# Kernel optimization log

Measured on AMD Instinct MI355X. Metric: run time of the kernel, lower is better.

Reference implementation:

```python
import jax, jax.numpy as jnp
import numpy as np

B = 512
C = 256
HEADS = 16
DH = 16
SIGMA = 1e-4  # GaussianNoise(0.0001)
LEAK = 0.2


def _axial_attn(x, Wq, Wkv, Wo, bo, axis):
    # x: [B, 8, 4, 5, C]; attend along `axis`, folding other dims into batch.
    xm = jnp.moveaxis(x, axis, -2)                      # [..., T, C]
    q = xm @ Wq                                          # [..., T, C]
    kv = xm @ Wkv                                        # [..., T, 2C]
    k, v = kv[..., :C], kv[..., C:]
    hshape = q.shape[:-1] + (HEADS, DH)
    q = q.reshape(hshape)
    k = k.reshape(hshape)
    v = v.reshape(hshape)
    dots = jnp.einsum('...thd,...shd->...hts', q, k) * (DH ** -0.5)
    attn = jax.nn.softmax(dots, axis=-1)
    o = jnp.einsum('...hts,...shd->...thd', attn, v).reshape(xm.shape)
    o = o @ Wo + bo
    return jnp.moveaxis(o, -2, axis)


def setup_inputs() -> dict:
    key = jax.random.key(0)
    ks = jax.random.split(key, 12)
    inp = {
        'x': jax.random.normal(ks[0], (B, 8, 4, 5), jnp.float32),
        'noise': jax.random.normal(ks[1], (B, 8, 4, 5, 1), jnp.float32),
        'rand': jax.random.uniform(ks[2], (B, 8, 4, 5, 1), jnp.float32),
        # encoder Linear(2, 256, bias=False), stored as [in, out]
        'W_enc': jax.random.normal(ks[3], (2, C), jnp.float32) * (2 ** -0.5),
        # axial positional embedding (sum of per-axis params == one full param)
        'pos_emb': jax.random.normal(ks[4], (8, 4, 5, C), jnp.float32) * 0.02,
        # 2 AxialAttention layers x 3 axes of SelfAttention params
        'Wq': jax.random.normal(ks[5], (2, 3, C, C), jnp.float32) * (C ** -0.5),
        'Wkv': jax.random.normal(ks[6], (2, 3, C, 2 * C), jnp.float32) * (C ** -0.5),
        'Wo': jax.random.normal(ks[7], (2, 3, C, C), jnp.float32) * (C ** -0.5),
        'bo': jnp.zeros((2, 3, C), jnp.float32),
        # decoder Linear(256, 1, bias=True)
        'Wd': jax.random.normal(ks[8], (C, 1), jnp.float32) * (C ** -0.5),
        'bd': jnp.zeros((1,), jnp.float32),
    }
    return inp


def reference(x, noise, rand, W_enc, pos_emb, Wq, Wkv, Wo, bo, Wd, bd):
    h = x[..., None] + SIGMA * noise                  # unsqueeze + GaussianNoise
    h = jnp.concatenate([h, rand], axis=-1)           # [B,8,4,5,2]
    h = jnp.tanh(h @ W_enc)                           # [B,8,4,5,256]
    h = h + pos_emb                                   # axial positional embedding
    for l in range(2):                                # two AxialAttention blocks
        h = (_axial_attn(h, Wq[l, 0], Wkv[l, 0], Wo[l, 0], bo[l, 0], 1)
             + _axial_attn(h, Wq[l, 1], Wkv[l, 1], Wo[l, 1], bo[l, 1], 2)
             + _axial_attn(h, Wq[l, 2], Wkv[l, 2], Wo[l, 2], bo[l, 2], 3))
        h = jnp.where(h >= 0, h, LEAK * h)            # LeakyReLU(0.2)
    out = jax.nn.sigmoid(h @ Wd + bd)                 # decoder Linear + Sigmoid
    return out[..., 0]                                # squeeze(-1) -> [B,8,4,5]
```

## Files before the change

### kernel.cpp

```cpp
#include <hip/hip_runtime.h>
#include <hip/hip_bf16.h>
#include <math.h>

#define NPOS 81920
#define CDIM 256
#define SIGMA 1e-4f
#define LEAK 0.2f

typedef __hip_bfloat16 bf16;
typedef __bf16 bf16x8 __attribute__((ext_vector_type(8)));
typedef float f32x4 __attribute__((ext_vector_type(4)));

__device__ __forceinline__ float bf2f(unsigned short u) {
    return __uint_as_float(((unsigned)u) << 16);
}
__device__ __forceinline__ unsigned short f2bfu(float f) {
    bf16 h = __float2bfloat16(f);
    return *reinterpret_cast<unsigned short*>(&h);
}

__global__ void encode_kernel(const float* __restrict__ x, const float* __restrict__ noise,
                              const float* __restrict__ rnd, const float* __restrict__ We,
                              const float* __restrict__ pe, bf16* __restrict__ H) {
    int p = blockIdx.x;
    int c = threadIdx.x;
    float a = x[p] + SIGMA * noise[p];
    float b = rnd[p];
    float z = a * We[c] + b * We[CDIM + c];
    z = fminf(15.f, fmaxf(-15.f, z));
    float e = __expf(2.f * z);
    float th = 1.f - 2.f / (e + 1.f);
    H[(size_t)p * CDIM + c] = __float2bfloat16(th + pe[(p % 160) * CDIM + c]);
}

__global__ void bias3_kernel(const float* __restrict__ bo, float* __restrict__ bsum) {
    int l = blockIdx.x, c = threadIdx.x;
    bsum[l * CDIM + c] = bo[l * 768 + c] + bo[l * 768 + 256 + c] + bo[l * 768 + 512 + c];
}

__global__ void pack_qkv_kernel(const float* __restrict__ Wq, const float* __restrict__ Wkv,
                                bf16* __restrict__ out) {
    int mat = blockIdx.x / 768;
    int n = blockIdx.x % 768;
    int k = threadIdx.x;
    float v = (n < 256) ? Wq[(size_t)mat * 65536 + (size_t)k * 256 + n]
                        : Wkv[(size_t)mat * 131072 + (size_t)k * 512 + (n - 256)];
    out[(size_t)blockIdx.x * 256 + k] = __float2bfloat16(v);
}
__global__ void pack_wo_kernel(const float* __restrict__ Wo, bf16* __restrict__ out) {
    int l = blockIdx.x / 256;
    int n = blockIdx.x % 256;
    int ck = threadIdx.x;
    for (int a = 0; a < 3; a++)
        out[(size_t)(l * 256 + n) * 768 + a * 256 + ck] =
            __float2bfloat16(Wo[(((size_t)(l * 3 + a)) * 256 + ck) * 256 + n]);
}

__global__ __launch_bounds__(256, 2) void step_kernel(
    const bf16* __restrict__ Hg, const bf16* __restrict__ Wqkv, bf16* __restrict__ QKV,
    const bf16* __restrict__ O, const bf16* __restrict__ WoTl, bf16* __restrict__ Hnw,
    const float* __restrict__ bias, int nW, int nMblk) {
    __shared__ __bf16 smem[32768];
    int tid = threadIdx.x;
    int wave = tid >> 6, lane = tid & 63;
    int quad = lane >> 4, m = lane & 15;

    if (blockIdx.x >= nW) {
        __bf16* As = smem;
        __bf16* Bs = smem + 8192;
        int bid = blockIdx.x - nW;
        int xcd = bid & 7, slot = bid >> 3;
        int g = slot / 9;
        int nb = slot - g * 9;
        int mb = xcd + 8 * g;
        int bm = mb * 128, bn = nb * 256;
        int wr = (wave >> 1) * 64, wc = (wave & 1) * 128;
        f32x4 acc[4][8] = {};

#define STAGE_G(buf, k0)                                                                       \
    {                                                                                          \
        _Pragma("unroll") for (int rep = 0; rep < 2; rep++) {                                  \
            int ch = rep * 256 + wave * 64 + lane;                                             \
            int row = ch >> 2, cc = ch & 3, gc = cc ^ ((row >> 1) & 3);                        \
            __builtin_amdgcn_global_load_lds(                                                  \
                (const __attribute__((address_space(1))) void*)(Hg + (size_t)(bm + row) * CDIM \
                                                                + (k0) + gc * 8),              \
                (__attribute__((address_space(3))) void*)(As + (buf) * 4096                    \
                                                          + (rep * 256 + wave * 64) * 8),      \
                16, 0, 0);                                                                     \
        }                                                                                      \
        _Pragma("unroll") for (int rep = 0; rep < 4; rep++) {                                  \
            int ch = rep * 256 + wave * 64 + lane;                                             \
            int row = ch >> 2, cc = ch & 3, gc = cc ^ ((row >> 1) & 3);                        \
            __builtin_amdgcn_global_load_lds(                                                  \
                (const __attribute__((address_space(1))) void*)(Wqkv + (size_t)(bn + row) * 256\
                                                                + (k0) + gc * 8),              \
                (__attribute__((address_space(3))) void*)(Bs + (buf) * 8192                    \
                                                          + (rep * 256 + wave * 64) * 8),      \
                16, 0, 0);                                                                     \
        }                                                                                      \
    }

        STAGE_G(0, 0);
#pragma unroll
        for (int it = 0; it < 8; it++) {
            __syncthreads();
            if (it < 7) STAGE_G((it + 1) & 1, (it + 1) * 32);
            const __bf16* Ab = As + (it & 1) * 4096;
            const __bf16* Bb = Bs + (it & 1) * 8192;
            bf16x8 af[4], bfr[8];
#pragma unroll
            for (int i = 0; i < 4; i++) {
                int r = wr + i * 16 + m;
                af[i] = *(const bf16x8*)(Ab + r * 32 + ((quad ^ ((r >> 1) & 3)) * 8));
            }
#pragma unroll
            for (int j = 0; j < 8; j++) {
                int r = wc + j * 16 + m;
                bfr[j] = *(const bf16x8*)(Bb + r * 32 + ((quad ^ ((r >> 1) & 3)) * 8));
            }
#pragma unroll
            for (int i = 0; i < 4; i++)
#pragma unroll
                for (int j = 0; j < 8; j++)
                    acc[i][j] = __builtin_amdgcn_mfma_f32_16x16x32_bf16(af[i], bfr[j], acc[i][j], 0, 0, 0);
        }
#undef STAGE_G

        __syncthreads();
        {
            unsigned short* ct = (unsigned short*)smem;
#pragma unroll
            for (int i = 0; i < 4; i++)
#pragma unroll
                for (int j = 0; j < 8; j++)
#pragma unroll
                    for (int r = 0; r < 4; r++) {
                        int row = wr + i * 16 + quad * 4 + r;
                        int col = wc + j * 16 + m;
                        ct[row * 256 + col] = f2bfu(acc[i][j][r]);
                    }
            __syncthreads();
#pragma unroll
            for (int p = 0; p < 16; p++) {
                int chunk = p * 256 + tid;
                int row = chunk >> 5, c8 = (chunk & 31) * 8;
                ulonglong2 v = *(const ulonglong2*)(ct + row * 256 + c8);
                *(ulonglong2*)((unsigned short*)QKV + (size_t)(bm + row) * 2304 + bn + c8) = v;
            }
        }
    } else {
        __bf16* As = smem;
        __bf16* Bs = smem + 16384;
        int bid = blockIdx.x;
        int xcd = bid & 7, slot = bid >> 3;
        int g = slot >> 1;
        int nb = slot & 1;
        int mb = xcd + 8 * g;
        int bm = mb * 128, bn = nb * 128;
        int wr = (wave >> 1) * 64, wc = (wave & 1) * 64;
        f32x4 acc[4][4] = {};

#define STAGE_W(buf, k0)                                                                       \
    {                                                                                          \
        _Pragma("unroll") for (int rep = 0; rep < 4; rep++) {                                  \
            int ch = rep * 256 + wave * 64 + lane;                                             \
            int row = ch >> 3, cc = ch & 7, gc = cc ^ (row & 7);                               \
            __builtin_amdgcn_global_load_lds(                                                  \
                (const __attribute__((address_space(1))) void*)(O + (size_t)(bm + row) * 768   \
                                                                + (k0) + gc * 8),              \
                (__attribute__((address_space(3))) void*)(As + (buf) * 8192                    \
                                                          + (rep * 256 + wave * 64) * 8),      \
                16, 0, 0);                                                                     \
        }                                                                                      \
        _Pragma("unroll") for (int rep = 0; rep < 4; rep++) {                                  \
            int ch = rep * 256 + wave * 64 + lane;                                             \
            int row = ch >> 3, cc = ch & 7, gc = cc ^ (row & 7);                               \
            __builtin_amdgcn_global_load_lds(                                                  \
                (const __attribute__((address_space(1))) void*)(WoTl + (size_t)(bn + row) * 768\
                                                                + (k0) + gc * 8),              \
                (__attribute__((address_space(3))) void*)(Bs + (buf) * 8192                    \
                                                          + (rep * 256 + wave * 64) * 8),      \
                16, 0, 0);                                                                     \
        }                                                                                      \
    }

        STAGE_W(0, 0);
#pragma unroll
        for (int it = 0; it < 12; it++) {
            __syncthreads();
            if (it < 11) STAGE_W((it + 1) & 1, (it + 1) * 64);
            const __bf16* Ab = As + (it & 1) * 8192;
            const __bf16* Bb = Bs + (it & 1) * 8192;
#pragma unroll
            for (int kk = 0; kk < 2; kk++) {
                bf16x8 af[4], bfr[4];
#pragma unroll
                for (int i = 0; i < 4; i++) {
                    int r = wr + i * 16 + m, cix = kk * 4 + quad;
                    af[i] = *(const bf16x8*)(Ab + r * 64 + ((cix ^ (r & 7)) * 8));
                }
#pragma unroll
                for (int j = 0; j < 4; j++) {
                    int r = wc + j * 16 + m, cix = kk * 4 + quad;
                    bfr[j] = *(const bf16x8*)(Bb + r * 64 + ((cix ^ (r & 7)) * 8));
                }
#pragma unroll
                for (int i = 0; i < 4; i++)
#pragma unroll
                    for (int j = 0; j < 4; j++)
                        acc[i][j] = __builtin_amdgcn_mfma_f32_16x16x32_bf16(af[i], bfr[j], acc[i][j], 0, 0, 0);
            }
        }
#undef STAGE_W

        __syncthreads();
        {
            unsigned short* ct = (unsigned short*)smem;
#pragma unroll
            for (int i = 0; i < 4; i++)
#pragma unroll
                for (int j = 0; j < 4; j++)
#pragma unroll
                    for (int r = 0; r < 4; r++) {
                        int row = wr + i * 16 + quad * 4 + r;
                        int lcol = wc + j * 16 + m;
                        float v = acc[i][j][r] + bias[bn + lcol];
                        v = v >= 0.f ? v : LEAK * v;
                        ct[row * 128 + lcol] = f2bfu(v);
                    }
            __syncthreads();
#pragma unroll
            for (int p = 0; p < 8; p++) {
                int chunk = p * 256 + tid;
                int row = chunk >> 4, c8 = (chunk & 15) * 8;
                ulonglong2 v = *(const ulonglong2*)(ct + row * 128 + c8);
                *(ulonglong2*)((unsigned short*)Hnw + (size_t)(bm + row) * CDIM + bn + c8) = v;
            }
        }
    }
}

template <int AXIS>
__device__ __forceinline__ void attn_axis(const bf16* __restrict__ QKV, bf16* __restrict__ O,
                                          int seq, int lane) {
    constexpr int T      = (AXIS == 0) ? 8 : (AXIS == 1) ? 4 : 5;
    constexpr int STRIDE = (AXIS == 0) ? 20 : (AXIS == 1) ? 5 : 1;
    int base;
    if (AXIS == 0)      { int b = seq / 20, r = seq % 20; base = b * 160 + r; }
    else if (AXIS == 1) { int b = seq / 40, r = seq % 40; base = b * 160 + (r / 5) * 20 + (r % 5); }
    else                { int b = seq / 32, r = seq % 32; base = b * 160 + r * 5; }

    float q[T][4], k[T][4], v[T][4];
#pragma unroll
    for (int t = 0; t < T; t++) {
        const unsigned short* rowp =
            (const unsigned short*)QKV + (size_t)(base + t * STRIDE) * 2304 + AXIS * 768 + lane * 4;
        ushort4 qu = *(const ushort4*)(rowp);
        ushort4 ku = *(const ushort4*)(rowp + 256);
        ushort4 vu = *(const ushort4*)(rowp + 512);
        q[t][0] = bf2f(qu.x); q[t][1] = bf2f(qu.y); q[t][2] = bf2f(qu.z); q[t][3] = bf2f(qu.w);
        k[t][0] = bf2f(ku.x); k[t][1] = bf2f(ku.y); k[t][2] = bf2f(ku.z); k[t][3] = bf2f(ku.w);
        v[t][0] = bf2f(vu.x); v[t][1] = bf2f(vu.y); v[t][2] = bf2f(vu.z); v[t][3] = bf2f(vu.w);
    }

#pragma unroll
    for (int t = 0; t < T; t++) {
        float sc[T];
#pragma unroll
        for (int s = 0; s < T; s++) {
            float p = q[t][0] * k[s][0] + q[t][1] * k[s][1] + q[t][2] * k[s][2] + q[t][3] * k[s][3];
            p += __shfl_xor(p, 1);
            p += __shfl_xor(p, 2);
            sc[s] = p * 0.25f;
        }
        float mx = sc[0];
#pragma unroll
        for (int s = 1; s < T; s++) mx = fmaxf(mx, sc[s]);
        float sum = 0.f;
#pragma unroll
        for (int s = 0; s < T; s++) { sc[s] = __expf(sc[s] - mx); sum += sc[s]; }
        float inv = 1.f / sum;
        float o0 = 0.f, o1 = 0.f, o2 = 0.f, o3 = 0.f;
#pragma unroll
        for (int s = 0; s < T; s++) {
            o0 += sc[s] * v[s][0]; o1 += sc[s] * v[s][1];
            o2 += sc[s] * v[s][2]; o3 += sc[s] * v[s][3];
        }
        ushort4 st;
        st.x = f2bfu(o0 * inv); st.y = f2bfu(o1 * inv);
        st.z = f2bfu(o2 * inv); st.w = f2bfu(o3 * inv);
        *(ushort4*)((unsigned short*)O + (size_t)(base + t * STRIDE) * 768 + AXIS * 256 + lane * 4) = st;
    }
}

__global__ __launch_bounds__(256) void attn_all(const bf16* __restrict__ QKV,
                                                bf16* __restrict__ O, int n0, int n1) {
    int wave = threadIdx.x >> 6, lane = threadIdx.x & 63;
    int blk = blockIdx.x;
    if (blk < n0)            attn_axis<0>(QKV, O, blk * 4 + wave, lane);
    else if (blk < n0 + n1)  attn_axis<1>(QKV, O, (blk - n0) * 4 + wave, lane);
    else                     attn_axis<2>(QKV, O, (blk - n0 - n1) * 4 + wave, lane);
}

__global__ void decode_kernel(const bf16* __restrict__ H, const float* __restrict__ Wd,
                              const float* __restrict__ bd, float* __restrict__ out) {
    int tid = threadIdx.x;
    int pos = blockIdx.x * 4 + (tid >> 6);
    int lane = tid & 63;
    float acc = 0.f;
#pragma unroll
    for (int q = 0; q < 4; q++) {
        int c = lane + q * 64;
        acc += __bfloat162float(H[(size_t)pos * CDIM + c]) * Wd[c];
    }
#pragma unroll
    for (int off = 32; off > 0; off >>= 1) acc += __shfl_down(acc, off);
    if (lane == 0) out[pos] = 1.f / (1.f + __expf(-(acc + bd[0])));
}

extern "C" void kernel_launch(void* const* d_in, const int* in_sizes, int n_in,
                              void* d_out, int out_size, void* d_ws, size_t ws_size,
                              hipStream_t stream) {
    const float* x     = (const float*)d_in[0];
    const float* noise = (const float*)d_in[1];
    const float* rnd   = (const float*)d_in[2];
    const float* We    = (const float*)d_in[3];
    const float* pe    = (const float*)d_in[4];
    const float* Wq    = (const float*)d_in[5];
    const float* Wkv   = (const float*)d_in[6];
    const float* Wo    = (const float*)d_in[7];
    const float* bo    = (const float*)d_in[8];
    const float* Wd    = (const float*)d_in[9];
    const float* bd    = (const float*)d_in[10];
    float* out = (float*)d_out;

    bf16* H0    = (bf16*)d_ws;
    bf16* H1    = H0 + (size_t)NPOS * CDIM;
    bf16* WqkvT = H1 + (size_t)NPOS * CDIM;
    bf16* WoT   = WqkvT + (size_t)2 * 2304 * 256;
    float* bsum = (float*)(WoT + (size_t)2 * 256 * 768);
    bf16* QKV   = (bf16*)(bsum + 512);

    size_t fixed = ((size_t)2 * NPOS * CDIM + (size_t)2 * 2304 * 256 + (size_t)2 * 256 * 768) * 2
                   + 512 * 4;
    int c = 4;
    while (c < 64 && fixed + (size_t)(NPOS / c) * (2304 + 768) * 2 > ws_size) c <<= 1;
    int mc = NPOS / c;
    bf16* O = QKV + (size_t)mc * 2304;
    bf16* Hbuf[3] = { H0, H1, H0 };

    pack_qkv_kernel<<<6 * 768, 256, 0, stream>>>(Wq, Wkv, WqkvT);
    pack_wo_kernel<<<2 * 256, 256, 0, stream>>>(Wo, WoT);
    bias3_kernel<<<2, 256, 0, stream>>>(bo, bsum);
    encode_kernel<<<NPOS, 256, 0, stream>>>(x, noise, rnd, We, pe, H0);

    int nMblk = mc / 128;
    int n0 = (mc / 160) * 20 / 4, n1 = (mc / 160) * 40 / 4, n2 = (mc / 160) * 32 / 4;
    int TT = 2 * c;

    for (int t = 0; t <= TT; t++) {
        int gG = (t < TT) ? nMblk * 9 : 0;
        int gW = (t >= 1) ? nMblk * 2 : 0;
        const bf16 *Hg = nullptr, *Wq_ = nullptr;
        if (gG) {
            int lg = t / c, cg = t % c;
            Hg = Hbuf[lg] + (size_t)cg * mc * CDIM;
            Wq_ = WqkvT + (size_t)lg * 2304 * 256;
        }
        const bf16* WoTl = nullptr; bf16* Hnw = nullptr; const float* bs = nullptr;
        if (gW) {
            int tw = t - 1, lw = tw / c, cw = tw % c;
            WoTl = WoT + (size_t)lw * 256 * 768;
            Hnw = Hbuf[lw + 1] + (size_t)cw * mc * CDIM;
            bs = bsum + lw * CDIM;
        }
        step_kernel<<<gG + gW, 256, 0, stream>>>(Hg, Wq_, QKV, O, WoTl, Hnw, bs, gW, nMblk);
        if (t < TT) attn_all<<<n0 + n1 + n2, 256, 0, stream>>>(QKV, O, n0, n1);
    }

    decode_kernel<<<NPOS / 4, 256, 0, stream>>>(Hbuf[2], Wd, bd, out);
}
```

Baseline: 675.5 us.

## Write QKV per axis in sequence-contiguous layout and swizzle epilogue LDS tiles

The QKV GEMM epilogue now scatters each output row into one of three per-axis buffers, ordered so that every attention sequence's tokens are contiguous with a 768-wide row. The attention kernel then reads consecutive rows instead of strided rows from a 2304-wide buffer. An XOR swizzle is also applied to the LDS staging tiles in both epilogues to reduce bank conflicts. The epilogue store becomes a scattered write with integer div/mod, and correctness relies on mc matching nMblk*128 and on chunk rows lining up with 160-row cells.

After: 721.7 us. +6.9%, slower.

```diff
diff --git a/kernel.cpp b/kernel.cpp
--- a/kernel.cpp
+++ b/kernel.cpp
@@ -138,15 +138,25 @@
                     for (int r = 0; r < 4; r++) {
                         int row = wr + i * 16 + quad * 4 + r;
                         int col = wc + j * 16 + m;
-                        ct[row * 256 + col] = f2bfu(acc[i][j][r]);
+                        ct[row * 256 + (col ^ (((row >> 2) & 3) << 4))] = f2bfu(acc[i][j][r]);
                     }
             __syncthreads();
+            int axis = nb / 3, colA = (nb % 3) * 256;
+            bf16* QA = QKV + (size_t)axis * (nMblk * 128) * 768;
 #pragma unroll
             for (int p = 0; p < 16; p++) {
                 int chunk = p * 256 + tid;
                 int row = chunk >> 5, c8 = (chunk & 31) * 8;
-                ulonglong2 v = *(const ulonglong2*)(ct + row * 256 + c8);
-                *(ulonglong2*)((unsigned short*)QKV + (size_t)(bm + row) * 2304 + bn + c8) = v;
+                ulonglong2 v = *(const ulonglong2*)(ct + row * 256
+                                                    + (c8 ^ (((row >> 2) & 3) << 4)));
+                int grow = bm + row;
+                int cell = grow / 160, r = grow % 160;
+                int off;
+                if (axis == 0)      off = (r % 20) * 8 + r / 20;
+                else if (axis == 1) off = ((r / 20) * 5 + (r % 5)) * 4 + (r % 20) / 5;
+                else                off = ((r / 20) * 4 + (r % 20) / 5) * 5 + (r % 5);
+                *(ulonglong2*)((unsigned short*)QA + (size_t)(cell * 160 + off) * 768
+                               + colA + c8) = v;
             }
         }
     } else {
@@ -227,14 +237,15 @@
                         int lcol = wc + j * 16 + m;
                         float v = acc[i][j][r] + bias[bn + lcol];
                         v = v >= 0.f ? v : LEAK * v;
-                        ct[row * 128 + lcol] = f2bfu(v);
+                        ct[row * 128 + (lcol ^ (((row >> 2) & 3) << 4))] = f2bfu(v);
                     }
             __syncthreads();
 #pragma unroll
             for (int p = 0; p < 8; p++) {
                 int chunk = p * 256 + tid;
                 int row = chunk >> 4, c8 = (chunk & 15) * 8;
-                ulonglong2 v = *(const ulonglong2*)(ct + row * 128 + c8);
+                ulonglong2 v = *(const ulonglong2*)(ct + row * 128
+                                                    + (c8 ^ (((row >> 2) & 3) << 4)));
                 *(ulonglong2*)((unsigned short*)Hnw + (size_t)(bm + row) * CDIM + bn + c8) = v;
             }
         }
@@ -242,20 +253,18 @@
 }
 
 template <int AXIS>
-__device__ __forceinline__ void attn_axis(const bf16* __restrict__ QKV, bf16* __restrict__ O,
+__device__ __forceinline__ void attn_axis(const bf16* __restrict__ QA, bf16* __restrict__ O,
                                           int seq, int lane) {
-    constexpr int T      = (AXIS == 0) ? 8 : (AXIS == 1) ? 4 : 5;
-    constexpr int STRIDE = (AXIS == 0) ? 20 : (AXIS == 1) ? 5 : 1;
-    int base;
-    if (AXIS == 0)      { int b = seq / 20, r = seq % 20; base = b * 160 + r; }
-    else if (AXIS == 1) { int b = seq / 40, r = seq % 40; base = b * 160 + (r / 5) * 20 + (r % 5); }
-    else                { int b = seq / 32, r = seq % 32; base = b * 160 + r * 5; }
-
+    constexpr int T  = (AXIS == 0) ? 8 : (AXIS == 1) ? 4 : 5;
+    constexpr int NS = (AXIS == 0) ? 20 : (AXIS == 1) ? 40 : 32;
+    int cell = seq / NS, sl = seq % NS;
+
+    const unsigned short* qb =
+        (const unsigned short*)QA + (size_t)(cell * 160 + sl * T) * 768 + lane * 4;
     float q[T][4], k[T][4], v[T][4];
 #pragma unroll
     for (int t = 0; t < T; t++) {
-        const unsigned short* rowp =
-            (const unsigned short*)QKV + (size_t)(base + t * STRIDE) * 2304 + AXIS * 768 + lane * 4;
+        const unsigned short* rowp = qb + t * 768;
         ushort4 qu = *(const ushort4*)(rowp);
         ushort4 ku = *(const ushort4*)(rowp + 256);
         ushort4 vu = *(const ushort4*)(rowp + 512);
@@ -290,17 +299,22 @@
         ushort4 st;
         st.x = f2bfu(o0 * inv); st.y = f2bfu(o1 * inv);
         st.z = f2bfu(o2 * inv); st.w = f2bfu(o3 * inv);
-        *(ushort4*)((unsigned short*)O + (size_t)(base + t * STRIDE) * 768 + AXIS * 256 + lane * 4) = st;
+        int lr;
+        if (AXIS == 0)      lr = t * 20 + sl;
+        else if (AXIS == 1) lr = (sl / 5) * 20 + (sl % 5) + t * 5;
+        else                lr = (sl / 4) * 20 + (sl % 4) * 5 + t;
+        *(ushort4*)((unsigned short*)O + (size_t)(cell * 160 + lr) * 768 + AXIS * 256 + lane * 4) = st;
     }
 }
 
 __global__ __launch_bounds__(256) void attn_all(const bf16* __restrict__ QKV,
-                                                bf16* __restrict__ O, int n0, int n1) {
+                                                bf16* __restrict__ O, int n0, int n1, int mc) {
     int wave = threadIdx.x >> 6, lane = threadIdx.x & 63;
     int blk = blockIdx.x;
     if (blk < n0)            attn_axis<0>(QKV, O, blk * 4 + wave, lane);
-    else if (blk < n0 + n1)  attn_axis<1>(QKV, O, (blk - n0) * 4 + wave, lane);
-    else                     attn_axis<2>(QKV, O, (blk - n0 - n1) * 4 + wave, lane);
+    else if (blk < n0 + n1)  attn_axis<1>(QKV + (size_t)mc * 768, O, (blk - n0) * 4 + wave, lane);
+    else                     attn_axis<2>(QKV + (size_t)2 * mc * 768, O,
+                                          (blk - n0 - n1) * 4 + wave, lane);
 }
 
 __global__ void decode_kernel(const bf16* __restrict__ H, const float* __restrict__ Wd,
@@ -376,7 +390,7 @@
             bs = bsum + lw * CDIM;
         }
         step_kernel<<<gG + gW, 256, 0, stream>>>(Hg, Wq_, QKV, O, WoTl, Hnw, bs, gW, nMblk);
-        if (t < TT) attn_all<<<n0 + n1 + n2, 256, 0, stream>>>(QKV, O, n0, n1);
+        if (t < TT) attn_all<<<n0 + n1 + n2, 256, 0, stream>>>(QKV, O, n0, n1, mc);
     }
 
     decode_kernel<<<NPOS / 4, 256, 0, stream>>>(Hbuf[2], Wd, bd, out);
```
